# Performance work log

Measured on AMD Instinct MI355X. Metric: run time of the kernel, lower is better.

## Reference

```python
import jax, jax.numpy as jnp
import numpy as np

H = 4096
NUM_HEADS = 32
D = 128
SEQ_LEN = 1024
CTX = 4096


def setup_inputs() -> dict:
    key = jax.random.key(0)
    k1, k2, k3, k4 = jax.random.split(key, 4)
    X = jax.random.normal(k1, (SEQ_LEN, H), dtype=jnp.float32)
    # Linear weight [out=3H, in=H]; scale ~1/sqrt(H) so attention logits are O(1)
    W = jax.random.normal(k2, (3 * H, H), dtype=jnp.float32) * (1.0 / np.sqrt(H))
    cache_K = jax.random.normal(k3, (1, CTX, NUM_HEADS, D), dtype=jnp.float32)
    cache_V = jax.random.normal(k4, (1, CTX, NUM_HEADS, D), dtype=jnp.float32)
    return {"X": X, "W": W, "cache_K": cache_K, "cache_V": cache_V}


def reference(X, W, cache_K, cache_V):
    seq_len, h = X.shape
    nh, d = cache_K.shape[2], cache_K.shape[3]
    # fused QKV projection (Linear, no bias): X @ W^T -> [seq_len, 3H]
    qkv = X @ W.T
    q, k, v = jnp.split(qkv, 3, axis=1)
    q = q.reshape(1, seq_len, nh, d)
    k = k.reshape(1, seq_len, nh, d)
    v = v.reshape(1, seq_len, nh, d)
    # concat KV cache along the sequence dim (cache_K[:, :P] with P = full cache)
    k_full = jnp.concatenate([cache_K, k], axis=1)  # [1, ctx+seq, nh, d]
    v_full = jnp.concatenate([cache_V, v], axis=1)
    scale = 1.0 / np.sqrt(d)
    # scores: [1, nh, seq_q, kv_len]
    scores = jnp.einsum("bqhd,bkhd->bhqk", q, k_full) * scale
    weights = jax.nn.softmax(scores, axis=-1)
    out = jnp.einsum("bhqk,bkhd->bqhd", weights, v_full)  # [1, seq, nh, d]
    return out.reshape(seq_len, h)
```

## Files before the change

kernel.cpp:

```cpp
#include <hip/hip_runtime.h>
#include <hip/hip_bf16.h>
#include <stdint.h>

#define H_DIM 4096
#define NH 32
#define HD 128
#define SEQ 1024
#define CTX 4096
#define KVL (CTX + SEQ)
#define W3H (3 * H_DIM)
#define ATTN_SCALE 0.08838834764831845f

typedef short short8 __attribute__((ext_vector_type(8)));
typedef float f32x4 __attribute__((ext_vector_type(4)));

#define GLOAD_LDS16(g, l)                                             \
  __builtin_amdgcn_global_load_lds(                                   \
      (const __attribute__((address_space(1))) void*)(g),             \
      (__attribute__((address_space(3))) void*)(l), 16, 0, 0)

__device__ __forceinline__ unsigned short f2b(float f) {
  union { float f; unsigned u; } v; v.f = f;
  return (unsigned short)((v.u + 0x7FFFu + ((v.u >> 16) & 1u)) >> 16);
}
__device__ __forceinline__ float b2f(unsigned short u) {
  union { unsigned u; float f; } v; v.u = ((unsigned)u) << 16;
  return v.f;
}

__global__ void k_cvt2(const float* __restrict__ X, const float* __restrict__ W,
                       unsigned short* __restrict__ Xb, unsigned short* __restrict__ Wb) {
  const int nx = SEQ * H_DIM / 4;
  const int nw = W3H * H_DIM / 4;
  int i = blockIdx.x * 256 + threadIdx.x;
  const float* s;
  unsigned short* d;
  int j;
  if (i < nx) { s = X; d = Xb; j = i; }
  else { j = i - nx; if (j >= nw) return; s = W; d = Wb; }
  float4 v = reinterpret_cast<const float4*>(s)[j];
  ushort4 o;
  o.x = f2b(v.x); o.y = f2b(v.y); o.z = f2b(v.z); o.w = f2b(v.w);
  reinterpret_cast<ushort4*>(d)[j] = o;
}

#define GBM 256
#define GBN 192
#define GBK 64
#define GNKT (H_DIM / GBK)
#define LBUF 57344
__global__ __launch_bounds__(512, 1) void k_gemm_qkv(
    const unsigned short* __restrict__ A,
    const unsigned short* __restrict__ B,
    unsigned short* __restrict__ C) {
  __shared__ __align__(16) char Lds[2 * LBUF];
  const int tid = threadIdx.x;
  const int lane = tid & 63;
  const int wid = tid >> 6;
  const int wm = wid >> 2;
  const int wn = wid & 3;
  const int lq = lane >> 4;
  const int lr = lane & 15;

  const int id = blockIdx.x;
  const int wg = (id & 7) * 32 + (id >> 3);
  const int bm = wg & 3;
  const int bn = wg >> 2;

  const unsigned short* Abase = A + (size_t)(bm * GBM) * H_DIM;
  const unsigned short* Bbase = B + (size_t)(bn * GBN) * H_DIM;
  const int sel = 8 * ((lane & 7) ^ (lane >> 3));
  const int srow = lane >> 3;

#define GA2(t, j0, b)                                                          \
  {                                                                            \
    _Pragma("unroll") for (int j = (j0); j < (j0) + 2; ++j) {                  \
      int c = wid + j * 8;                                                     \
      GLOAD_LDS16(Abase + (size_t)(c * 8 + srow) * H_DIM + (t) * GBK + sel,    \
                  Lds + (b) * LBUF + c * 1024);                                \
    }                                                                          \
  }
#define GB2(t, j0, b)                                                          \
  {                                                                            \
    _Pragma("unroll") for (int j = (j0); j < (j0) + 2; ++j) {                  \
      int c = wid + j * 8;                                                     \
      GLOAD_LDS16(Bbase + (size_t)(c * 8 + srow) * H_DIM + (t) * GBK + sel,    \
                  Lds + (b) * LBUF + 32768 + c * 1024);                        \
    }                                                                          \
  }
#define GB1(t, j0, b)                                                          \
  {                                                                            \
    int c = wid + (j0) * 8;                                                    \
    GLOAD_LDS16(Bbase + (size_t)(c * 8 + srow) * H_DIM + (t) * GBK + sel,      \
                Lds + (b) * LBUF + 32768 + c * 1024);                          \
  }

  f32x4 acc[8][3] = {};

#define GPHASE(T, q)                                                           \
  {                                                                            \
    const int cb_ = ((T) & 1) * LBUF;                                          \
    short8 af[2][2];                                                           \
    _Pragma("unroll") for (int mm = 0; mm < 2; ++mm)                           \
      _Pragma("unroll") for (int kk = 0; kk < 2; ++kk)                         \
        af[mm][kk] = *reinterpret_cast<const short8*>(                         \
            Lds + cb_ + (wm * 128 + ((q) * 2 + mm) * 16 + lr) * 128 +          \
            16 * ((kk * 4 + lq) ^ (lr & 7)));                                  \
    if ((q) == 0) {                                                            \
      _Pragma("unroll") for (int n = 0; n < 3; ++n)                            \
        _Pragma("unroll") for (int kk = 0; kk < 2; ++kk)                       \
          bfr[n][kk] = *reinterpret_cast<const short8*>(                       \
              Lds + cb_ + 32768 + (wn * 48 + n * 16 + lr) * 128 +              \
              16 * ((kk * 4 + lq) ^ (lr & 7)));                                \
    }                                                                          \
    if ((q) == 0 && (T) + 1 < GNKT) GA2((T) + 1, 0, ((T) + 1) & 1);            \
    if ((q) == 1 && (T) + 1 < GNKT) GA2((T) + 1, 2, ((T) + 1) & 1);            \
    if ((q) == 2 && (T) + 2 < GNKT) GB2((T) + 2, 0, (T) & 1);                  \
    if ((q) == 3 && (T) + 2 < GNKT) GB1((T) + 2, 2, (T) & 1);                  \
    if ((q) == 3) {                                                            \
      if ((T) + 2 < GNKT) {                                                    \
        asm volatile("s_waitcnt vmcnt(3)" ::: "memory");                       \
      } else {                                                                 \
        asm volatile("s_waitcnt vmcnt(0)" ::: "memory");                       \
      }                                                                        \
    }                                                                          \
    __builtin_amdgcn_sched_barrier(0);                                         \
    __builtin_amdgcn_s_barrier();                                              \
    asm volatile("s_waitcnt lgkmcnt(0)" ::: "memory");                         \
    __builtin_amdgcn_sched_barrier(0);                                         \
    __builtin_amdgcn_s_setprio(1);                                             \
    _Pragma("unroll") for (int kk = 0; kk < 2; ++kk)                           \
      _Pragma("unroll") for (int mm = 0; mm < 2; ++mm)                         \
        _Pragma("unroll") for (int n = 0; n < 3; ++n)                          \
          acc[(q) * 2 + mm][n] = __builtin_amdgcn_mfma_f32_16x16x32_bf16(      \
              af[mm][kk], bfr[n][kk], acc[(q) * 2 + mm][n], 0, 0, 0);          \
    __builtin_amdgcn_s_setprio(0);                                             \
    __builtin_amdgcn_sched_barrier(0);                                         \
    __builtin_amdgcn_s_barrier();                                              \
    __builtin_amdgcn_sched_barrier(0);                                         \
  }

  GA2(0, 0, 0);
  GA2(0, 2, 0);
  GB2(0, 0, 0);
  GB1(0, 2, 0);
  GB2(1, 0, 1);
  GB1(1, 2, 1);
  asm volatile("s_waitcnt vmcnt(3)" ::: "memory");
  __builtin_amdgcn_sched_barrier(0);
  __builtin_amdgcn_s_barrier();
  __builtin_amdgcn_sched_barrier(0);

  for (int T = 0; T < GNKT; ++T) {
    short8 bfr[3][2];
    GPHASE(T, 0);
    GPHASE(T, 1);
    GPHASE(T, 2);
    GPHASE(T, 3);
  }

  const int r0 = bm * GBM + wm * 128 + lq * 4;
  const int c0 = bn * GBN + wn * 48 + lr;
#pragma unroll
  for (int m = 0; m < 8; ++m)
#pragma unroll
    for (int n = 0; n < 3; ++n)
#pragma unroll
      for (int r = 0; r < 4; ++r)
        C[(size_t)(r0 + m * 16 + r) * W3H + c0 + n * 16] = f2b(acc[m][n][r]);
#undef GA2
#undef GB2
#undef GB1
#undef GPHASE
}

__global__ void k_build_k(const float* __restrict__ cK, const unsigned short* __restrict__ QKV,
                          unsigned short* __restrict__ Kb) {
  int idx = (blockIdx.x * 256 + threadIdx.x) * 4;
  if (idx >= NH * KVL * HD) return;
  int h = idx / (KVL * HD);
  int rem = idx % (KVL * HD);
  int kv = rem / HD;
  int d = rem % HD;
  ushort4 o;
  if (kv < CTX) {
    float4 v = *reinterpret_cast<const float4*>(cK + ((size_t)kv * NH + h) * HD + d);
    o.x = f2b(v.x); o.y = f2b(v.y); o.z = f2b(v.z); o.w = f2b(v.w);
  } else {
    o = *reinterpret_cast<const ushort4*>(QKV + (size_t)(kv - CTX) * W3H + H_DIM + h * HD + d);
  }
  *reinterpret_cast<ushort4*>(Kb + idx) = o;
}

__global__ void k_build_vt(const float* __restrict__ cV, const unsigned short* __restrict__ QKV,
                           unsigned short* __restrict__ Vt) {
  __shared__ unsigned short T[HD][66];
  const int h = blockIdx.y;
  const int kt = blockIdx.x;
  const int t = threadIdx.x;
#pragma unroll
  for (int e = 0; e < 8; ++e) {
    int idx = (t + e * 256) * 4;
    int kvl = idx >> 7;
    int d = idx & 127;
    int kv = kt * 64 + kvl;
    unsigned short a, b, c, w;
    if (kv < CTX) {
      float4 v = *reinterpret_cast<const float4*>(cV + ((size_t)kv * NH + h) * HD + d);
      a = f2b(v.x); b = f2b(v.y); c = f2b(v.z); w = f2b(v.w);
    } else {
      ushort4 u = *reinterpret_cast<const ushort4*>(QKV + (size_t)(kv - CTX) * W3H + 2 * H_DIM + h * HD + d);
      a = u.x; b = u.y; c = u.z; w = u.w;
    }
    T[d][kvl] = a; T[d + 1][kvl] = b; T[d + 2][kvl] = c; T[d + 3][kvl] = w;
  }
  __syncthreads();
#pragma unroll
  for (int e = 0; e < 8; ++e) {
    int idx = (t + e * 256) * 4;
    int d = idx >> 6;
    int kv0 = idx & 63;
    ushort4 o;
    o.x = T[d][kv0]; o.y = T[d][kv0 + 1]; o.z = T[d][kv0 + 2]; o.w = T[d][kv0 + 3];
    *reinterpret_cast<ushort4*>(Vt + ((size_t)h * HD + d) * KVL + kt * 64 + kv0) = o;
  }
}

#define PKV(x) ((((x) & 32)) | (((x) & 12) << 1) | (((x) & 16) >> 2) | ((x) & 3))
#define KVT 64
#define NT (KVL / KVT)
#define NT2 (NT / 2)
__global__ __launch_bounds__(256, 2) void k_attn(
    const unsigned short* __restrict__ QKV,
    const unsigned short* __restrict__ Kb,
    const unsigned short* __restrict__ Vt,
    float* __restrict__ A0,
    float* __restrict__ A1,
    float* __restrict__ Mp,
    float* __restrict__ Lp) {
  __shared__ unsigned short Ks[2][KVT * HD];
  __shared__ unsigned short Vs[2][KVT * HD];
  const int tid = threadIdx.x, lane = tid & 63, wid = tid >> 6;
  const int g = lane >> 4;
  const int qi = lane & 15;
  const int id = blockIdx.x;
  const int xcd = id & 7, slot = id >> 3;
  const int h = xcd * 4 + (slot >> 4);
  const int rem = slot & 15;
  const int qt = rem >> 1;
  const int split = rem & 1;
  const int kt0 = split * NT2;
  const int q0 = qt * 128 + wid * 32;

  short8 qf[2][4];
#pragma unroll
  for (int hf = 0; hf < 2; ++hf)
#pragma unroll
    for (int c = 0; c < 4; ++c) {
      short8 q = *reinterpret_cast<const short8*>(
          QKV + (size_t)(q0 + hf * 16 + qi) * W3H + h * HD + c * 32 + g * 8);
      short8 t;
#pragma unroll
      for (int j = 0; j < 8; ++j) t[j] = (short)f2b(b2f((unsigned short)q[j]) * ATTN_SCALE);
      qf[hf][c] = t;
    }

  float m_r[2] = {-1e30f, -1e30f}, l_r[2] = {0.f, 0.f};
  f32x4 acc_o[2][8] = {};

  const char* Kh = (const char*)(Kb + (size_t)h * KVL * HD);
  const char* Vh = (const char*)(Vt + (size_t)h * HD * KVL);

#define STAGE_K(t, b)                                                          \
  {                                                                            \
    _Pragma("unroll") for (int i = 0; i < 4; ++i) {                            \
      int c = wid * 4 + i;                                                     \
      int krow = c * 4 + (lane >> 4);                             \
      int kglob = PKV(krow);                       \
      int klcb = (16 * (lane & 15)) ^ ((krow & 7) << 4);                       \
      GLOAD_LDS16(Kh + (size_t)((t) * KVT + kglob) * 256 + klcb,               \
                  (char*)Ks[b] + c * 1024);                                    \
    }                                                                          \
  }
#define STAGE_V(t, b)                                                          \
  {                                                                            \
    _Pragma("unroll") for (int i = 0; i < 4; ++i) {                            \
      int c = wid * 4 + i;                                                     \
      int vrow = c * 8 + (lane >> 3);                                          \
      int vlcb = (16 * (lane & 7)) ^ ((vrow & 7) << 4);                        \
      GLOAD_LDS16(Vh + (size_t)vrow * (KVL * 2) + (size_t)(t) * 128 + vlcb,    \
                  (char*)Vs[b] + c * 1024);                                    \
    }                                                                          \
  }
#define QKT(buf, S)                                                            \
  {                                                                            \
    _Pragma("unroll") for (int n = 0; n < 4; ++n) {                            \
      S[0][n] = (f32x4){0.f, 0.f, 0.f, 0.f};                                   \
      S[1][n] = (f32x4){0.f, 0.f, 0.f, 0.f};                                   \
    }                                                                          \
    __builtin_amdgcn_s_setprio(1);                                             \
    _Pragma("unroll") for (int n = 0; n < 4; ++n) {                            \
      int row = n * 16 + qi;                                                   \
      _Pragma("unroll") for (int c = 0; c < 4; ++c) {                          \
        int cb = (c * 32 + g * 8) * 2;                                         \
        short8 kf = *reinterpret_cast<const short8*>(                          \
            (const char*)Ks[buf] + row * 256 + (cb ^ ((row & 7) << 4)));       \
        S[0][n] = __builtin_amdgcn_mfma_f32_16x16x32_bf16(kf, qf[0][c], S[0][n], 0, 0, 0); \
        S[1][n] = __builtin_amdgcn_mfma_f32_16x16x32_bf16(kf, qf[1][c], S[1][n], 0, 0, 0); \
      }                                                                        \
    }                                                                          \
    __builtin_amdgcn_s_setprio(0);                                             \
  }

#define SMPV(S, vb)                                                            \
  {                                                                            \
    float p[2][4][4];                                                          \
    int okv = 1;                                                               \
    float tmax[2];                                                             \
    _Pragma("unroll") for (int hf = 0; hf < 2; ++hf) {                         \
      float t0 = S[hf][0][0];                                                  \
      _Pragma("unroll") for (int n = 0; n < 4; ++n)                            \
        _Pragma("unroll") for (int r = 0; r < 4; ++r)                          \
          t0 = fmaxf(t0, S[hf][n][r]);                                         \
      t0 = fmaxf(t0, __shfl_xor(t0, 16, 64));                                  \
      t0 = fmaxf(t0, __shfl_xor(t0, 32, 64));                                  \
      tmax[hf] = t0;                                                           \
      okv &= (t0 <= m_r[hf] + 8.0f);                                           \
    }                                                                          \
    if (!__all(okv)) {                                                         \
      _Pragma("unroll") for (int hf = 0; hf < 2; ++hf) {                       \
        float mn = fmaxf(m_r[hf], tmax[hf]);                                   \
        float alpha = __expf(m_r[hf] - mn);                                    \
        l_r[hf] *= alpha;                                                      \
        m_r[hf] = mn;                                                          \
        _Pragma("unroll") for (int nd = 0; nd < 8; ++nd) acc_o[hf][nd] *= alpha; \
      }                                                                        \
    }                                                                          \
    _Pragma("unroll") for (int hf = 0; hf < 2; ++hf) {                         \
      float sum = 0.f;                                                         \
      _Pragma("unroll") for (int n = 0; n < 4; ++n)                            \
        _Pragma("unroll") for (int r = 0; r < 4; ++r) {                        \
          p[hf][n][r] = __expf(S[hf][n][r] - m_r[hf]);                         \
          sum += p[hf][n][r];                                                  \
        }                                                                      \
      l_r[hf] += sum;     \
    }                                                                          \
    unsigned pr[2][4][2];                                                      \
    _Pragma("unroll") for (int hf = 0; hf < 2; ++hf)                           \
      _Pragma("unroll") for (int n = 0; n < 4; ++n)                            \
        _Pragma("unroll") for (int rr = 0; rr < 2; ++rr) {                     \
          union { __hip_bfloat162 b; unsigned u; } cv;                         \
          cv.b = __float22bfloat162_rn(                                        \
              make_float2(p[hf][n][2 * rr], p[hf][n][2 * rr + 1]));            \
          pr[hf][n][rr] = cv.u;                                                \
        }                                                                      \
    _Pragma("unroll") for (int kc = 0; kc < 2; ++kc) {                         \
      short8 pv[2];                                                            \
      _Pragma("unroll") for (int hf = 0; hf < 2; ++hf) {                       \
        union { unsigned u[4]; short8 s8; } u;                                 \
        u.u[0] = pr[hf][2 * kc][0];                                            \
        u.u[1] = pr[hf][2 * kc][1];                                            \
        u.u[2] = pr[hf][2 * kc + 1][0];                                        \
        u.u[3] = pr[hf][2 * kc + 1][1];                                        \
        pv[hf] = u.s8;                                                         \
      }                                                                        \
      __builtin_amdgcn_s_setprio(1);                                           \
      _Pragma("unroll") for (int nd = 0; nd < 8; ++nd) {                       \
        int row = nd * 16 + qi;                                                \
        int cb = kc * 64 + g * 16;                                             \
        short8 vf = *reinterpret_cast<const short8*>(                          \
            (const char*)Vs[vb] + row * 128 + (cb ^ ((row & 7) << 4)));        \
        acc_o[0][nd] = __builtin_amdgcn_mfma_f32_16x16x32_bf16(vf, pv[0], acc_o[0][nd], 0, 0, 0); \
        acc_o[1][nd] = __builtin_amdgcn_mfma_f32_16x16x32_bf16(vf, pv[1], acc_o[1][nd], 0, 0, 0); \
      }                                                                        \
      __builtin_amdgcn_s_setprio(0);                                           \
    }                                                                          \
  }

#define BODY(t, SC, SN)                                                        \
  {                                                                            \
    const int cur = (t) & 1;                                                   \
    if ((t) + 2 < NT2) STAGE_K(kt0 + (t) + 2, cur);                            \
    if ((t) + 1 < NT2) QKT(cur ^ 1, SN);                                       \
    SMPV(SC, cur);                                                             \
    __syncthreads();                                                           \
    if ((t) + 2 < NT2) STAGE_V(kt0 + (t) + 2, cur);                            \
  }

  STAGE_K(kt0, 0);
  STAGE_V(kt0, 0);
  STAGE_K(kt0 + 1, 1);
  STAGE_V(kt0 + 1, 1);
  __syncthreads();

  f32x4 sA[2][4], sB[2][4];
  QKT(0, sA);

  for (int tt = 0; tt < NT2; tt += 2) {
    BODY(tt, sA, sB);
    BODY(tt + 1, sB, sA);
  }

#pragma unroll
  for (int hf = 0; hf < 2; ++hf) {
    l_r[hf] += __shfl_xor(l_r[hf], 16, 64);
    l_r[hf] += __shfl_xor(l_r[hf], 32, 64);
  }

  float* Op = split ? A1 : A0;
#pragma unroll
  for (int hf = 0; hf < 2; ++hf) {
    float* orow = Op + (size_t)(q0 + hf * 16 + qi) * H_DIM + h * HD;
#pragma unroll
    for (int nd = 0; nd < 8; ++nd)
      *reinterpret_cast<float4*>(orow + nd * 16 + g * 4) =
          *reinterpret_cast<const float4*>(&acc_o[hf][nd]);
    if (g == 0) {
      int q = q0 + hf * 16 + qi;
      Mp[split * (NH * SEQ) + h * SEQ + q] = m_r[hf];
      Lp[split * (NH * SEQ) + h * SEQ + q] = l_r[hf];
    }
  }
#undef STAGE_K
#undef STAGE_V
#undef QKT
#undef SMPV
#undef BODY
}

__global__ void k_combine(const float* __restrict__ A1, const float* __restrict__ Mp,
                          const float* __restrict__ Lp, float* __restrict__ out) {
  int i4 = blockIdx.x * 256 + threadIdx.x;
  int q = i4 >> 10;
  int c4 = i4 & 1023;
  int h = c4 >> 5;
  float m0 = Mp[h * SEQ + q], m1 = Mp[NH * SEQ + h * SEQ + q];
  float l0 = Lp[h * SEQ + q], l1 = Lp[NH * SEQ + h * SEQ + q];
  float M = fmaxf(m0, m1);
  float w0 = __expf(m0 - M), w1 = __expf(m1 - M);
  float inv = 1.0f / (w0 * l0 + w1 * l1);
  float4 a0 = reinterpret_cast<const float4*>(out)[i4];
  float4 a1 = reinterpret_cast<const float4*>(A1)[i4];
  float4 o;
  o.x = (w0 * a0.x + w1 * a1.x) * inv;
  o.y = (w0 * a0.y + w1 * a1.y) * inv;
  o.z = (w0 * a0.z + w1 * a1.z) * inv;
  o.w = (w0 * a0.w + w1 * a1.w) * inv;
  reinterpret_cast<float4*>(out)[i4] = o;
}

extern "C" void kernel_launch(void* const* d_in, const int* in_sizes, int n_in,
                              void* d_out, int out_size, void* d_ws, size_t ws_size,
                              hipStream_t stream) {
  const float* X = (const float*)d_in[0];
  const float* W = (const float*)d_in[1];
  const float* cK = (const float*)d_in[2];
  const float* cV = (const float*)d_in[3];
  float* out = (float*)d_out;
  char* ws = (char*)d_ws;

  unsigned short* Xb = (unsigned short*)(ws);
  float* Mp = (float*)(ws);
  float* Lp = (float*)(ws + (256 << 10));
  unsigned short* QKVb = (unsigned short*)(ws + ((size_t)8 << 20));
  unsigned short* Wb = (unsigned short*)(ws + ((size_t)32 << 20));
  unsigned short* Kb = (unsigned short*)(ws + ((size_t)32 << 20));
  unsigned short* Vt = (unsigned short*)(ws + ((size_t)72 << 20));
  float* A1 = (float*)(ws + ((size_t)112 << 20));

  int ncvt = (SEQ * H_DIM + W3H * H_DIM) / 4;
  k_cvt2<<<(ncvt + 255) / 256, 256, 0, stream>>>(X, W, Xb, Wb);

  k_gemm_qkv<<<(SEQ / GBM) * (W3H / GBN), 512, 0, stream>>>(Xb, Wb, QKVb);

  k_build_k<<<(NH * KVL * HD / 4) / 256, 256, 0, stream>>>(cK, QKVb, Kb);
  dim3 gv(KVL / 64, NH);
  k_build_vt<<<gv, 256, 0, stream>>>(cV, QKVb, Vt);

  k_attn<<<SEQ / 128 * NH * 2, 256, 0, stream>>>(QKVb, Kb, Vt, out, A1, Mp, Lp);
  k_combine<<<(SEQ * H_DIM / 4) / 256, 256, 0, stream>>>(A1, Mp, Lp, out);
}
```

Measured before the change: 373.0 us.

## Replace software-pipelined QK/softmax-PV loop with a simple sequential per-tile loop

Removes the software pipeline that computed QK^T for the next tile while the current tile's softmax and PV ran, and that staged K ahead of the barrier. Each iteration now runs QK^T, softmax and PV for the current tile in order, then syncs and stages the K and V tiles two steps ahead. This frees the second score register set and simplifies scheduling, at the cost of losing overlap between MFMA work on scores and softmax exp work.

```diff
diff --git a/kernel.cpp b/kernel.cpp
--- a/kernel.cpp
+++ b/kernel.cpp
@@ -292,100 +292,6 @@
                   (char*)Vs[b] + c * 1024);                                    \
     }                                                                          \
   }
-#define QKT(buf, S)                                                            \
-  {                                                                            \
-    _Pragma("unroll") for (int n = 0; n < 4; ++n) {                            \
-      S[0][n] = (f32x4){0.f, 0.f, 0.f, 0.f};                                   \
-      S[1][n] = (f32x4){0.f, 0.f, 0.f, 0.f};                                   \
-    }                                                                          \
-    __builtin_amdgcn_s_setprio(1);                                             \
-    _Pragma("unroll") for (int n = 0; n < 4; ++n) {                            \
-      int row = n * 16 + qi;                                                   \
-      _Pragma("unroll") for (int c = 0; c < 4; ++c) {                          \
-        int cb = (c * 32 + g * 8) * 2;                                         \
-        short8 kf = *reinterpret_cast<const short8*>(                          \
-            (const char*)Ks[buf] + row * 256 + (cb ^ ((row & 7) << 4)));       \
-        S[0][n] = __builtin_amdgcn_mfma_f32_16x16x32_bf16(kf, qf[0][c], S[0][n], 0, 0, 0); \
-        S[1][n] = __builtin_amdgcn_mfma_f32_16x16x32_bf16(kf, qf[1][c], S[1][n], 0, 0, 0); \
-      }                                                                        \
-    }                                                                          \
-    __builtin_amdgcn_s_setprio(0);                                             \
-  }
-
-#define SMPV(S, vb)                                                            \
-  {                                                                            \
-    float p[2][4][4];                                                          \
-    int okv = 1;                                                               \
-    float tmax[2];                                                             \
-    _Pragma("unroll") for (int hf = 0; hf < 2; ++hf) {                         \
-      float t0 = S[hf][0][0];                                                  \
-      _Pragma("unroll") for (int n = 0; n < 4; ++n)                            \
-        _Pragma("unroll") for (int r = 0; r < 4; ++r)                          \
-          t0 = fmaxf(t0, S[hf][n][r]);                                         \
-      t0 = fmaxf(t0, __shfl_xor(t0, 16, 64));                                  \
-      t0 = fmaxf(t0, __shfl_xor(t0, 32, 64));                                  \
-      tmax[hf] = t0;                                                           \
-      okv &= (t0 <= m_r[hf] + 8.0f);                                           \
-    }                                                                          \
-    if (!__all(okv)) {                                                         \
-      _Pragma("unroll") for (int hf = 0; hf < 2; ++hf) {                       \
-        float mn = fmaxf(m_r[hf], tmax[hf]);                                   \
-        float alpha = __expf(m_r[hf] - mn);                                    \
-        l_r[hf] *= alpha;                                                      \
-        m_r[hf] = mn;                                                          \
-        _Pragma("unroll") for (int nd = 0; nd < 8; ++nd) acc_o[hf][nd] *= alpha; \
-      }                                                                        \
-    }                                                                          \
-    _Pragma("unroll") for (int hf = 0; hf < 2; ++hf) {                         \
-      float sum = 0.f;                                                         \
-      _Pragma("unroll") for (int n = 0; n < 4; ++n)                            \
-        _Pragma("unroll") for (int r = 0; r < 4; ++r) {                        \
-          p[hf][n][r] = __expf(S[hf][n][r] - m_r[hf]);                         \
-          sum += p[hf][n][r];                                                  \
-        }                                                                      \
-      l_r[hf] += sum;     \
-    }                                                                          \
-    unsigned pr[2][4][2];                                                      \
-    _Pragma("unroll") for (int hf = 0; hf < 2; ++hf)                           \
-      _Pragma("unroll") for (int n = 0; n < 4; ++n)                            \
-        _Pragma("unroll") for (int rr = 0; rr < 2; ++rr) {                     \
-          union { __hip_bfloat162 b; unsigned u; } cv;                         \
-          cv.b = __float22bfloat162_rn(                                        \
-              make_float2(p[hf][n][2 * rr], p[hf][n][2 * rr + 1]));            \
-          pr[hf][n][rr] = cv.u;                                                \
-        }                                                                      \
-    _Pragma("unroll") for (int kc = 0; kc < 2; ++kc) {                         \
-      short8 pv[2];                                                            \
-      _Pragma("unroll") for (int hf = 0; hf < 2; ++hf) {                       \
-        union { unsigned u[4]; short8 s8; } u;                                 \
-        u.u[0] = pr[hf][2 * kc][0];                                            \
-        u.u[1] = pr[hf][2 * kc][1];                                            \
-        u.u[2] = pr[hf][2 * kc + 1][0];                                        \
-        u.u[3] = pr[hf][2 * kc + 1][1];                                        \
-        pv[hf] = u.s8;                                                         \
-      }                                                                        \
-      __builtin_amdgcn_s_setprio(1);                                           \
-      _Pragma("unroll") for (int nd = 0; nd < 8; ++nd) {                       \
-        int row = nd * 16 + qi;                                                \
-        int cb = kc * 64 + g * 16;                                             \
-        short8 vf = *reinterpret_cast<const short8*>(                          \
-            (const char*)Vs[vb] + row * 128 + (cb ^ ((row & 7) << 4)));        \
-        acc_o[0][nd] = __builtin_amdgcn_mfma_f32_16x16x32_bf16(vf, pv[0], acc_o[0][nd], 0, 0, 0); \
-        acc_o[1][nd] = __builtin_amdgcn_mfma_f32_16x16x32_bf16(vf, pv[1], acc_o[1][nd], 0, 0, 0); \
-      }                                                                        \
-      __builtin_amdgcn_s_setprio(0);                                           \
-    }                                                                          \
-  }
-
-#define BODY(t, SC, SN)                                                        \
-  {                                                                            \
-    const int cur = (t) & 1;                                                   \
-    if ((t) + 2 < NT2) STAGE_K(kt0 + (t) + 2, cur);                            \
-    if ((t) + 1 < NT2) QKT(cur ^ 1, SN);                                       \
-    SMPV(SC, cur);                                                             \
-    __syncthreads();                                                           \
-    if ((t) + 2 < NT2) STAGE_V(kt0 + (t) + 2, cur);                            \
-  }
 
   STAGE_K(kt0, 0);
   STAGE_V(kt0, 0);
@@ -393,12 +299,110 @@
   STAGE_V(kt0 + 1, 1);
   __syncthreads();
 
-  f32x4 sA[2][4], sB[2][4];
-  QKT(0, sA);
-
-  for (int tt = 0; tt < NT2; tt += 2) {
-    BODY(tt, sA, sB);
-    BODY(tt + 1, sB, sA);
+  for (int kt = 0; kt < NT2; ++kt) {
+    const int cur = kt & 1;
+
+    f32x4 s[2][4];
+#pragma unroll
+    for (int n = 0; n < 4; ++n) {
+      s[0][n] = (f32x4){0.f, 0.f, 0.f, 0.f};
+      s[1][n] = (f32x4){0.f, 0.f, 0.f, 0.f};
+    }
+    __builtin_amdgcn_s_setprio(1);
+#pragma unroll
+    for (int n = 0; n < 4; ++n) {
+      int row = n * 16 + qi;
+#pragma unroll
+      for (int c = 0; c < 4; ++c) {
+        int cb = (c * 32 + g * 8) * 2;
+        short8 kf = *reinterpret_cast<const short8*>(
+            (const char*)Ks[cur] + row * 256 + (cb ^ ((row & 7) << 4)));
+        s[0][n] = __builtin_amdgcn_mfma_f32_16x16x32_bf16(kf, qf[0][c], s[0][n], 0, 0, 0);
+        s[1][n] = __builtin_amdgcn_mfma_f32_16x16x32_bf16(kf, qf[1][c], s[1][n], 0, 0, 0);
+      }
+    }
+    __builtin_amdgcn_s_setprio(0);
+
+    float p[2][4][4];
+    int okv = 1;
+    float tmax[2];
+#pragma unroll
+    for (int hf = 0; hf < 2; ++hf) {
+      float t0 = s[hf][0][0];
+#pragma unroll
+      for (int n = 0; n < 4; ++n)
+#pragma unroll
+        for (int r = 0; r < 4; ++r) t0 = fmaxf(t0, s[hf][n][r]);
+      t0 = fmaxf(t0, __shfl_xor(t0, 16, 64));
+      t0 = fmaxf(t0, __shfl_xor(t0, 32, 64));
+      tmax[hf] = t0;
+      okv &= (t0 <= m_r[hf] + 8.0f);
+    }
+    if (!__all(okv)) {
+#pragma unroll
+      for (int hf = 0; hf < 2; ++hf) {
+        float mn = fmaxf(m_r[hf], tmax[hf]);
+        float alpha = __expf(m_r[hf] - mn);
+        l_r[hf] *= alpha;
+        m_r[hf] = mn;
+#pragma unroll
+        for (int nd = 0; nd < 8; ++nd) acc_o[hf][nd] *= alpha;
+      }
+    }
+#pragma unroll
+    for (int hf = 0; hf < 2; ++hf) {
+      float sum = 0.f;
+#pragma unroll
+      for (int n = 0; n < 4; ++n)
+#pragma unroll
+        for (int r = 0; r < 4; ++r) {
+          p[hf][n][r] = __expf(s[hf][n][r] - m_r[hf]);
+          sum += p[hf][n][r];
+        }
+      l_r[hf] += sum;
+    }
+
+    unsigned pr[2][4][2];
+#pragma unroll
+    for (int hf = 0; hf < 2; ++hf)
+#pragma unroll
+      for (int n = 0; n < 4; ++n)
+#pragma unroll
+        for (int rr = 0; rr < 2; ++rr) {
+          union { __hip_bfloat162 b; unsigned u; } cv;
+          cv.b = __float22bfloat162_rn(make_float2(p[hf][n][2 * rr], p[hf][n][2 * rr + 1]));
+          pr[hf][n][rr] = cv.u;
+        }
+#pragma unroll
+    for (int kc = 0; kc < 2; ++kc) {
+      short8 pv[2];
+#pragma unroll
+      for (int hf = 0; hf < 2; ++hf) {
+        union { unsigned u[4]; short8 s8; } u;
+        u.u[0] = pr[hf][2 * kc][0];
+        u.u[1] = pr[hf][2 * kc][1];
+        u.u[2] = pr[hf][2 * kc + 1][0];
+        u.u[3] = pr[hf][2 * kc + 1][1];
+        pv[hf] = u.s8;
+      }
+      __builtin_amdgcn_s_setprio(1);
+#pragma unroll
+      for (int nd = 0; nd < 8; ++nd) {
+        int row = nd * 16 + qi;
+        int cb = kc * 64 + g * 16;
+        short8 vf = *reinterpret_cast<const short8*>(
+            (const char*)Vs[cur] + row * 128 + (cb ^ ((row & 7) << 4)));
+        acc_o[0][nd] = __builtin_amdgcn_mfma_f32_16x16x32_bf16(vf, pv[0], acc_o[0][nd], 0, 0, 0);
+        acc_o[1][nd] = __builtin_amdgcn_mfma_f32_16x16x32_bf16(vf, pv[1], acc_o[1][nd], 0, 0, 0);
+      }
+      __builtin_amdgcn_s_setprio(0);
+    }
+
+    __syncthreads();
+    if (kt + 2 < NT2) {
+      STAGE_K(kt0 + kt + 2, cur);
+      STAGE_V(kt0 + kt + 2, cur);
+    }
   }
 
 #pragma unroll
@@ -423,9 +427,6 @@
   }
 #undef STAGE_K
 #undef STAGE_V
-#undef QKT
-#undef SMPV
-#undef BODY
 }
 
 __global__ void k_combine(const float* __restrict__ A1, const float* __restrict__ Mp,
```

New measurement: 301.8 us. 1.24x faster.
